# Kernel optimization log

Hardware: AMD Instinct MI355X
Metric: run time of the kernel (lower is better)

Reference implementation:

```python
import jax, jax.numpy as jnp
import numpy as np

B, T, D = 4, 2048, 1024

def layer_norm(x, gamma, bias):
    # NOTE: faithfully reproduces the source's (buggy) LN: x - mu/sqrt(var), unbiased var
    mu = jnp.mean(x, axis=-1, keepdims=True)
    var = jnp.var(x, axis=-1, ddof=1, keepdims=True)
    return (x - mu / jnp.sqrt(var)) * gamma + bias

def setup_inputs() -> dict:
    key = jax.random.key(0)
    ks = jax.random.split(key, 8)
    scale = 1.0 / np.sqrt(D)
    return {
        'x': jax.random.normal(ks[0], (B, T, D), dtype=jnp.float32),
        'gamma1': jnp.ones((D,), jnp.float32),
        'beta1': jnp.zeros((D,), jnp.float32),
        'w_q': jax.random.uniform(ks[1], (D, D), jnp.float32, -scale, scale),
        'w_k': jax.random.uniform(ks[2], (D, D), jnp.float32, -scale, scale),
        'w_v': jax.random.uniform(ks[3], (D, D), jnp.float32, -scale, scale),
        'gamma2': jnp.ones((D,), jnp.float32),
        'beta2': jnp.zeros((D,), jnp.float32),
        'W1': jax.random.uniform(ks[4], (D, D), jnp.float32, -scale, scale),
        'b1': jnp.zeros((D,), jnp.float32),
        'W2': jax.random.uniform(ks[5], (D, D), jnp.float32, -scale, scale),
        'b2': jnp.zeros((D,), jnp.float32),
    }

def reference(x, gamma1, beta1, w_q, w_k, w_v, gamma2, beta2, W1, b1, W2, b2):
    d_model = x.shape[-1]
    t = x.shape[1]
    h = layer_norm(x, gamma1, beta1)
    q = jnp.einsum('btk,kd->btd', h, w_q)
    k = jnp.einsum('btk,kd->btd', h, w_k)
    v = jnp.einsum('btk,kd->btd', h, w_v)
    scale = 1.0 / jnp.sqrt(jnp.asarray(d_model, x.dtype))
    causal = jnp.tril(jnp.ones((t, t), dtype=bool))
    mask = jnp.where(causal, 0.0, -jnp.inf).astype(x.dtype)
    scores = jnp.einsum('bqd,bkd->bqk', q, k) * scale + mask
    attn = jax.nn.softmax(scores, axis=-1)
    y = jnp.einsum('bqt,btd->bqd', attn, v) + x
    h2 = layer_norm(y, gamma2, beta2)
    out = jnp.maximum(h2 @ W1 + b1, 0.0) @ W2 + b2
    return out + y
```

## Files before the change

kernel.cpp:

```cpp
#include <hip/hip_runtime.h>
#include <hip/hip_bf16.h>
#include <math.h>

using bf16 = __hip_bfloat16;

static constexpr int Bn = 4;
static constexpr int Tn = 2048;
static constexpr int Dn = 1024;

typedef __attribute__((ext_vector_type(8))) short bf16x8;
typedef __attribute__((ext_vector_type(4))) float f32x4;

__device__ __forceinline__ float ldf(float v) { return v; }
__device__ __forceinline__ float ldf(bf16 v) { return __bfloat162float(v); }
__device__ __forceinline__ bf16 f2b(float v) { return __float2bfloat16(v); }
__device__ __forceinline__ float b2f(short s) {
    return __uint_as_float(((unsigned)(unsigned short)s) << 16);
}
__device__ __forceinline__ short f2bs(float v) {
    bf16 t = __float2bfloat16(v);
    return *reinterpret_cast<short*>(&t);
}

template <typename T> __device__ __forceinline__ T from_float(float v);
template <> __device__ __forceinline__ float from_float<float>(float v) { return v; }
template <> __device__ __forceinline__ bf16 from_float<bf16>(float v) { return f2b(v); }

__device__ __forceinline__ void load4(const float* p, float* v) {
    const float4 t = *(const float4*)p;
    v[0] = t.x; v[1] = t.y; v[2] = t.z; v[3] = t.w;
}
__device__ __forceinline__ void load4(const bf16* p, float* v) {
    const short4 t = *(const short4*)p;
    v[0] = b2f(t.x); v[1] = b2f(t.y); v[2] = b2f(t.z); v[3] = b2f(t.w);
}

__device__ __forceinline__ void async_copy16(const bf16* g, bf16* l) {
    __builtin_amdgcn_global_load_lds(
        (const __attribute__((address_space(1))) void*)g,
        (__attribute__((address_space(3))) void*)l,
        16, 0, 0);
}

template <int BM, int BN, int MINW, int EPI, typename OutT, typename ResT, bool RELU>
__global__ __launch_bounds__(256, MINW) void gemm_nt(
    const bf16* __restrict__ A, const bf16* __restrict__ Bm,
    OutT* __restrict__ C, const float* __restrict__ bias,
    const ResT* __restrict__ res, bf16* __restrict__ vtp,
    float* __restrict__ rowsum,
    int M, int N, int K, int lda, int ldb, int ldc,
    long sA, long sB, long sC, long sR, int mode)
{
    const int bm = blockIdx.x, bn = blockIdx.y, bz = blockIdx.z;
    if (mode == 1 && bn * BN > bm * BM + (BM - 1)) return;
    const int kend = bm * BM + BM;
    const int kmax = (mode == 2) ? (kend < K ? kend : K) : K;

    const bf16* Ab = A + (size_t)bz * sA;
    const bf16* Bb = Bm + (size_t)bz * sB;

    constexpr int WROWS = BM / 64;
    constexpr int WCOLS = 4 / WROWS;
    constexpr int TM = 64;
    constexpr int TN = BN / WCOLS;
    constexpr int MT = TM / 16;
    constexpr int NT = TN / 16;
    constexpr int nA = BM / 16;
    constexpr int nB = BN / 16;
    constexpr int TSTR = 132;
    constexpr int STAGE = 2 * (BM + BN) * 32;
    constexpr int SME = (EPI == 1 && BM * TSTR > STAGE) ? BM * TSTR : STAGE;

    __shared__ __align__(16) bf16 smem[SME];
    bf16* As = smem;
    bf16* Bs = smem + 2 * BM * 32;

    const int tid = threadIdx.x;
    const int wave = tid >> 6;
    const int lane = tid & 63;
    const int wm = wave / WCOLS;
    const int wn = wave % WCOLS;

    f32x4 acc[MT][NT] = {};

    const int lr = lane >> 2;
    const int lc = (lane & 3) * 8;
    const bf16* gAc[nA / 4]; bf16* lAc[nA / 4];
    const bf16* gBc[nB / 4]; bf16* lBc[nB / 4];
#pragma unroll
    for (int i = 0; i < nA / 4; ++i) {
        const int c = wave + 4 * i;
        gAc[i] = Ab + (size_t)(bm * BM + c * 16 + lr) * lda + lc;
        lAc[i] = &As[c * 512];
    }
#pragma unroll
    for (int i = 0; i < nB / 4; ++i) {
        const int c = wave + 4 * i;
        gBc[i] = Bb + (size_t)(bn * BN + c * 16 + lr) * ldb + lc;
        lBc[i] = &Bs[c * 512];
    }

    const int arow = lane & 15;
    const int kq = (lane >> 4) * 8;

    for (int k0 = 0; k0 < kmax; k0 += 64) {
#pragma unroll
        for (int hh = 0; hh < 2; ++hh) {
#pragma unroll
            for (int i = 0; i < nA / 4; ++i)
                async_copy16(gAc[i] + k0 + 32 * hh, lAc[i] + hh * (BM * 32));
#pragma unroll
            for (int i = 0; i < nB / 4; ++i)
                async_copy16(gBc[i] + k0 + 32 * hh, lBc[i] + hh * (BN * 32));
        }
        __syncthreads();

#pragma unroll
        for (int hh = 0; hh < 2; ++hh) {
            const bf16* Ah = As + hh * (BM * 32);
            const bf16* Bh = Bs + hh * (BN * 32);
            bf16x8 af[MT], bfm[NT];
#pragma unroll
            for (int t = 0; t < MT; ++t)
                af[t] = *(const bf16x8*)&Ah[(wm * TM + t * 16 + arow) * 32 + kq];
#pragma unroll
            for (int t = 0; t < NT; ++t)
                bfm[t] = *(const bf16x8*)&Bh[(wn * TN + t * 16 + arow) * 32 + kq];
#pragma unroll
            for (int mt = 0; mt < MT; ++mt)
#pragma unroll
                for (int nt = 0; nt < NT; ++nt)
                    acc[mt][nt] = __builtin_amdgcn_mfma_f32_16x16x32_bf16(
                        af[mt], bfm[nt], acc[mt][nt], 0, 0, 0);
        }
        __syncthreads();
    }

    const int rowBase = bm * BM + wm * TM;
    const int colBase = bn * BN + wn * TN;
    const int qrow = (lane >> 4) * 4;
    const int ccol = lane & 15;

    if (EPI == 1 && bn * BN >= 2048) {
        bf16* tt = smem;
#pragma unroll
        for (int mt = 0; mt < MT; ++mt) {
            const int tl = wm * TM + mt * 16 + qrow;
#pragma unroll
            for (int nt = 0; nt < NT; ++nt) {
                const int dl = wn * TN + nt * 16 + ccol;
                short4 o;
                o.x = f2bs(acc[mt][nt][0]);
                o.y = f2bs(acc[mt][nt][1]);
                o.z = f2bs(acc[mt][nt][2]);
                o.w = f2bs(acc[mt][nt][3]);
                *(short4*)&tt[dl * TSTR + tl] = o;
            }
        }
        __syncthreads();
        const int dl = tid >> 1;
        const int th = (tid & 1) * 64;
        const int dg = bn * BN - 2048 + dl;
        const int b = (bm * BM) >> 11;
        const int tin = (bm * BM) & (Tn - 1);
        bf16* dst = vtp + ((size_t)b * Dn + dg) * Tn + tin + th;
        const bf16* srcl = &tt[dl * TSTR + th];
#pragma unroll
        for (int i = 0; i < 16; ++i)
            ((short4*)dst)[i] = ((const short4*)srcl)[i];
        return;
    }

    if (EPI == 2) {
        OutT* Cb = C + (size_t)bz * sC;
        float* rsb = rowsum + (size_t)bz * Tn;
        const float scale = 0.03125f;
#pragma unroll
        for (int mt = 0; mt < MT; ++mt) {
            float rsv[4] = {0.f, 0.f, 0.f, 0.f};
#pragma unroll
            for (int nt = 0; nt < NT; ++nt) {
                const int cc = colBase + nt * 16 + ccol;
#pragma unroll
                for (int r = 0; r < 4; ++r) {
                    const int rr = rowBase + mt * 16 + qrow + r;
                    float e = 0.0f;
                    if (cc <= rr) {
                        const short es = f2bs(__expf(acc[mt][nt][r] * scale));
                        Cb[(size_t)rr * ldc + cc] = *(const bf16*)&es;
                        e = b2f(es);
                    } else {
                        Cb[(size_t)rr * ldc + cc] = from_float<OutT>(0.0f);
                    }
                    rsv[r] += e;
                }
            }
#pragma unroll
            for (int r = 0; r < 4; ++r) {
                float v = rsv[r];
                v += __shfl_xor(v, 1);
                v += __shfl_xor(v, 2);
                v += __shfl_xor(v, 4);
                v += __shfl_xor(v, 8);
                if (ccol == 0)
                    atomicAdd(rsb + rowBase + mt * 16 + qrow + r, v);
            }
        }
        return;
    }

    OutT* Cb = C + (size_t)bz * sC;
    const ResT* Rb = res ? (res + (size_t)bz * sR) : nullptr;
    const float* rsb = (EPI == 3) ? (rowsum + (size_t)bz * Tn) : nullptr;
#pragma unroll
    for (int mt = 0; mt < MT; ++mt) {
        float inv4[4];
        if (EPI == 3) {
#pragma unroll
            for (int r = 0; r < 4; ++r)
                inv4[r] = 1.0f / rsb[rowBase + mt * 16 + qrow + r];
        }
#pragma unroll
        for (int nt = 0; nt < NT; ++nt) {
            const int cc = colBase + nt * 16 + ccol;
            const float bv = bias ? bias[cc] : 0.0f;
#pragma unroll
            for (int r = 0; r < 4; ++r) {
                const int rr = rowBase + mt * 16 + qrow + r;
                float v = acc[mt][nt][r];
                if (EPI == 3) v *= inv4[r];
                v += bv;
                if (RELU) v = fmaxf(v, 0.0f);
                if (Rb) v += ldf(Rb[(size_t)rr * ldc + cc]);
                Cb[(size_t)rr * ldc + cc] = from_float<OutT>(v);
            }
        }
    }
}

template <typename InT>
__device__ __forceinline__ void ln_row(
    const InT* __restrict__ xr, const float* __restrict__ gamma,
    const float* __restrict__ beta, bf16* __restrict__ orow, int tid)
{
    const int j = tid * 4;
    float v[4];
    load4(xr + j, v);
    float s = v[0] + v[1] + v[2] + v[3];
    float sq = v[0] * v[0] + v[1] * v[1] + v[2] * v[2] + v[3] * v[3];
#pragma unroll
    for (int o = 32; o > 0; o >>= 1) {
        s += __shfl_down(s, o);
        sq += __shfl_down(sq, o);
    }
    __shared__ float red[2][4];
    const int lane = tid & 63, w = tid >> 6;
    if (lane == 0) { red[0][w] = s; red[1][w] = sq; }
    __syncthreads();
    s  = red[0][0] + red[0][1] + red[0][2] + red[0][3];
    sq = red[1][0] + red[1][1] + red[1][2] + red[1][3];
    const float mean = s / (float)Dn;
    const float var = (sq - s * s / (float)Dn) / (float)(Dn - 1);
    const float coef = mean * rsqrtf(var);

    const float4 g = *(const float4*)(gamma + j);
    const float4 be = *(const float4*)(beta + j);
    short4 o;
    o.x = f2bs((v[0] - coef) * g.x + be.x);
    o.y = f2bs((v[1] - coef) * g.y + be.y);
    o.z = f2bs((v[2] - coef) * g.z + be.z);
    o.w = f2bs((v[3] - coef) * g.w + be.w);
    *(short4*)(orow + j) = o;
}

template <typename InT>
__global__ __launch_bounds__(256) void ln_kernel(
    const InT* __restrict__ x, const float* __restrict__ gamma,
    const float* __restrict__ beta, bf16* __restrict__ out)
{
    const int row = blockIdx.x;
    ln_row(x + (size_t)row * Dn, gamma, beta, out + (size_t)row * Dn, threadIdx.x);
}

struct WPtrs { const float* p[5]; };

__global__ __launch_bounds__(256) void prep_kernel(
    WPtrs wp, bf16* __restrict__ wdst, float* __restrict__ rowsum,
    const float* __restrict__ x, const float* __restrict__ gamma1,
    const float* __restrict__ beta1, bf16* __restrict__ h)
{
    const int bx = blockIdx.x;
    if (bx < 5120) {
        __shared__ bf16 tile[32][33];
        const int z = bx >> 10;
        const int t = bx & 1023;
        const float* src = wp.p[z];
        bf16* d = wdst + (size_t)z * Dn * Dn;
        const int c0 = (t & 31) * 32, r0 = (t >> 5) * 32;
        const int tx = threadIdx.x & 31;
        const int ty = threadIdx.x >> 5;
#pragma unroll
        for (int dy = 0; dy < 32; dy += 8)
            tile[ty + dy][tx] = f2b(src[(size_t)(r0 + ty + dy) * Dn + (c0 + tx)]);
        __syncthreads();
#pragma unroll
        for (int dy = 0; dy < 32; dy += 8)
            d[(size_t)(c0 + ty + dy) * Dn + (r0 + tx)] = tile[tx][ty + dy];
    } else if (bx < 5128) {
        const int idx = (bx - 5120) * 1024 + (int)threadIdx.x;
        const int base = (bx - 5120) * 1024;
#pragma unroll
        for (int i = 0; i < 4; ++i) rowsum[base + i * 256 + threadIdx.x] = 0.0f;
        (void)idx;
    } else {
        const int row = bx - 5128;
        ln_row(x + (size_t)row * Dn, gamma1, beta1, h + (size_t)row * Dn, threadIdx.x);
    }
}

extern "C" void kernel_launch(void* const* d_in, const int* in_sizes, int n_in,
                              void* d_out, int out_size, void* d_ws, size_t ws_size,
                              hipStream_t stream) {
    const float* x      = (const float*)d_in[0];
    const float* gamma1 = (const float*)d_in[1];
    const float* beta1  = (const float*)d_in[2];
    const float* w_q    = (const float*)d_in[3];
    const float* w_k    = (const float*)d_in[4];
    const float* w_v    = (const float*)d_in[5];
    const float* gamma2 = (const float*)d_in[6];
    const float* beta2  = (const float*)d_in[7];
    const float* W1     = (const float*)d_in[8];
    const float* b1     = (const float*)d_in[9];
    const float* W2     = (const float*)d_in[10];
    const float* b2     = (const float*)d_in[11];
    float* out = (float*)d_out;

    char* ws = (char*)d_ws;
    size_t off = 0;
    auto alloc = [&](size_t bytes) {
        char* p = ws + off;
        off += (bytes + 255) & ~(size_t)255;
        return p;
    };
    const size_t BT = (size_t)Bn * Tn;
    bf16* h    = (bf16*)alloc(BT * Dn * 2);
    bf16* qk   = (bf16*)alloc(BT * 2 * Dn * 2);
    bf16* vt   = (bf16*)alloc(BT * Dn * 2);
    bf16* wbuf = (bf16*)alloc((size_t)5 * Dn * Dn * 2);
    bf16* S    = (bf16*)alloc((size_t)Bn * Tn * Tn * 2);
    bf16* y    = (bf16*)alloc(BT * Dn * 2);
    float* rowsum = (float*)alloc((size_t)Bn * Tn * 4);
    bf16* h2   = h;
    bf16* mid  = qk;

    const dim3 blk(256);
    const long TD  = (long)Tn * Dn;
    const long TT  = (long)Tn * Tn;
    const long TD2 = (long)Tn * 2 * Dn;

    WPtrs wp; wp.p[0] = w_q; wp.p[1] = w_k; wp.p[2] = w_v; wp.p[3] = W1; wp.p[4] = W2;
    prep_kernel<<<dim3(5128 + (unsigned)BT, 1, 1), blk, 0, stream>>>(
        wp, wbuf, rowsum, x, gamma1, beta1, h);

    gemm_nt<128, 128, 4, 1, bf16, float, false><<<dim3(64, 24, 1), blk, 0, stream>>>(
        h, wbuf, qk, nullptr, nullptr, vt, nullptr,
        (int)BT, 3 * Dn, Dn, Dn, Dn, 2 * Dn, 0, 0, 0, 0, 0);

    gemm_nt<128, 128, 4, 2, bf16, float, false><<<dim3(16, 16, Bn), blk, 0, stream>>>(
        qk, qk + 1024, S, nullptr, nullptr, nullptr, rowsum,
        Tn, Tn, Dn, 2 * Dn, 2 * Dn, Tn, TD2, TD2, TT, 0, 1);

    gemm_nt<128, 128, 4, 3, bf16, float, false><<<dim3(16, 8, Bn), blk, 0, stream>>>(
        S, vt, y, nullptr, x, nullptr, rowsum,
        Tn, Dn, Tn, Tn, Tn, Dn, TT, TD, TD, TD, 2);

    ln_kernel<bf16><<<dim3((unsigned)BT), blk, 0, stream>>>(y, gamma2, beta2, h2);

    gemm_nt<128, 128, 4, 0, bf16, float, true><<<dim3(64, 8, 1), blk, 0, stream>>>(
        h2, wbuf + (size_t)3 * Dn * Dn, mid, b1, nullptr, nullptr, nullptr,
        (int)BT, Dn, Dn, Dn, Dn, Dn, 0, 0, 0, 0, 0);

    gemm_nt<128, 128, 4, 0, float, bf16, false><<<dim3(64, 8, 1), blk, 0, stream>>>(
        mid, wbuf + (size_t)4 * Dn * Dn, out, b2, y, nullptr, nullptr,
        (int)BT, Dn, Dn, Dn, Dn, Dn, 0, 0, 0, 0, 0);
}
```

Baseline: 353.5 us.

## Split QKV projection into 256x256 triple-buffered QK GEMM and transposed V GEMM

Replaces the single fused QKV GEMM, whose epilogue transposed V through shared memory, with two launches. A new 512-thread 256x256-tile kernel computes Q and K using a triple-buffered async global-to-LDS pipeline, split MFMA phases and priority hints. V^T is produced directly by a second GEMM with swapped operands (W_v^T times h per batch), so the transpose epilogue and its extra shared memory are removed. This adds a launch and relies on the hand-written wait counts and barriers in the new pipeline being correct.

```diff
diff --git a/kernel.cpp b/kernel.cpp
--- a/kernel.cpp
+++ b/kernel.cpp
@@ -40,6 +40,129 @@
         (const __attribute__((address_space(1))) void*)g,
         (__attribute__((address_space(3))) void*)l,
         16, 0, 0);
+}
+
+__global__ __launch_bounds__(512, 2) void gemm8p(
+    const bf16* __restrict__ A, const bf16* __restrict__ Bm,
+    bf16* __restrict__ C, int K, int lda, int ldb, int ldc)
+{
+    constexpr int BM = 256, BN = 256, BK = 32;
+    constexpr int BUFE = (BM + BN) * BK;
+    __shared__ __align__(16) bf16 smem[3 * BUFE];
+
+    const int bm = blockIdx.x, bn = blockIdx.y;
+    const int tid = threadIdx.x;
+    const int wave = tid >> 6;
+    const int lane = tid & 63;
+    const int wm = wave >> 2;
+    const int wn = wave & 3;
+    const int lr = lane >> 2;
+    const int lc = (lane & 3) * 8;
+    const int arow = lane & 15;
+    const int kq = (lane >> 4) * 8;
+
+    const int NK = K / BK;
+
+    const bf16* gA0 = A + (size_t)(bm * BM + wave * 16 + lr) * lda + lc;
+    const bf16* gA1 = A + (size_t)(bm * BM + (wave + 8) * 16 + lr) * lda + lc;
+    const bf16* gB0 = Bm + (size_t)(bn * BN + wave * 16 + lr) * ldb + lc;
+    const bf16* gB1 = Bm + (size_t)(bn * BN + (wave + 8) * 16 + lr) * ldb + lc;
+
+    f32x4 acc[8][4] = {};
+
+    {
+        bf16* As0 = smem;
+        bf16* Bs0 = smem + BM * BK;
+        bf16* As1 = smem + BUFE;
+        bf16* Bs1 = smem + BUFE + BM * BK;
+        async_copy16(gA0, As0 + wave * 512);
+        async_copy16(gA1, As0 + (wave + 8) * 512);
+        async_copy16(gB0, Bs0 + wave * 512);
+        async_copy16(gB1, Bs0 + (wave + 8) * 512);
+        async_copy16(gA0 + BK, As1 + wave * 512);
+        async_copy16(gA1 + BK, As1 + (wave + 8) * 512);
+        async_copy16(gB0 + BK, Bs1 + wave * 512);
+        async_copy16(gB1 + BK, Bs1 + (wave + 8) * 512);
+    }
+    asm volatile("s_waitcnt vmcnt(4)" ::: "memory");
+    __builtin_amdgcn_s_barrier();
+
+    int cb = 0;
+    int sb = 2;
+    for (int kt = 0; kt < NK; ++kt) {
+        const bf16* As = smem + cb * BUFE;
+        const bf16* Bs = As + BM * BK;
+        const bool st = (kt + 2) < NK;
+        const int koff = (kt + 2) * BK;
+
+        bf16x8 af[8], bf0[2];
+#pragma unroll
+        for (int mt = 0; mt < 8; ++mt)
+            af[mt] = *(const bf16x8*)&As[(wm * 8 + mt) * 512 + arow * 32 + kq];
+#pragma unroll
+        for (int nt = 0; nt < 2; ++nt)
+            bf0[nt] = *(const bf16x8*)&Bs[(wn * 4 + nt) * 512 + arow * 32 + kq];
+        if (st) {
+            bf16* Ad = smem + sb * BUFE;
+            async_copy16(gA0 + koff, Ad + wave * 512);
+            async_copy16(gA1 + koff, Ad + (wave + 8) * 512);
+        }
+        __builtin_amdgcn_s_barrier();
+        asm volatile("s_waitcnt lgkmcnt(0)" ::: "memory");
+        __builtin_amdgcn_sched_barrier(0);
+        __builtin_amdgcn_s_setprio(1);
+#pragma unroll
+        for (int mt = 0; mt < 8; ++mt)
+#pragma unroll
+            for (int nt = 0; nt < 2; ++nt)
+                acc[mt][nt] = __builtin_amdgcn_mfma_f32_16x16x32_bf16(
+                    af[mt], bf0[nt], acc[mt][nt], 0, 0, 0);
+        __builtin_amdgcn_s_setprio(0);
+        __builtin_amdgcn_s_barrier();
+
+        bf16x8 bf1[2];
+#pragma unroll
+        for (int nt = 0; nt < 2; ++nt)
+            bf1[nt] = *(const bf16x8*)&Bs[(wn * 4 + 2 + nt) * 512 + arow * 32 + kq];
+        if (st) {
+            bf16* Bd = smem + sb * BUFE + BM * BK;
+            async_copy16(gB0 + koff, Bd + wave * 512);
+            async_copy16(gB1 + koff, Bd + (wave + 8) * 512);
+        }
+        __builtin_amdgcn_s_barrier();
+        asm volatile("s_waitcnt lgkmcnt(0)" ::: "memory");
+        __builtin_amdgcn_sched_barrier(0);
+        __builtin_amdgcn_s_setprio(1);
+#pragma unroll
+        for (int mt = 0; mt < 8; ++mt)
+#pragma unroll
+            for (int nt = 0; nt < 2; ++nt)
+                acc[mt][2 + nt] = __builtin_amdgcn_mfma_f32_16x16x32_bf16(
+                    af[mt], bf1[nt], acc[mt][2 + nt], 0, 0, 0);
+        __builtin_amdgcn_s_setprio(0);
+        if (st) asm volatile("s_waitcnt vmcnt(4)" ::: "memory");
+        else    asm volatile("s_waitcnt vmcnt(0)" ::: "memory");
+        __builtin_amdgcn_s_barrier();
+
+        cb = (cb + 1 == 3) ? 0 : cb + 1;
+        sb = (sb + 1 == 3) ? 0 : sb + 1;
+    }
+
+    const int row0 = bm * BM + wm * 128;
+    const int col0 = bn * BN + wn * 64;
+    const int qrow = (lane >> 4) * 4;
+    const int ccol = lane & 15;
+#pragma unroll
+    for (int mt = 0; mt < 8; ++mt)
+#pragma unroll
+        for (int nt = 0; nt < 4; ++nt) {
+            const int cc = col0 + nt * 16 + ccol;
+#pragma unroll
+            for (int r = 0; r < 4; ++r) {
+                const int rr = row0 + mt * 16 + qrow + r;
+                C[(size_t)rr * ldc + cc] = f2b(acc[mt][nt][r]);
+            }
+        }
 }
 
 template <int BM, int BN, int MINW, int EPI, typename OutT, typename ResT, bool RELU>
@@ -67,11 +190,9 @@
     constexpr int NT = TN / 16;
     constexpr int nA = BM / 16;
     constexpr int nB = BN / 16;
-    constexpr int TSTR = 132;
     constexpr int STAGE = 2 * (BM + BN) * 32;
-    constexpr int SME = (EPI == 1 && BM * TSTR > STAGE) ? BM * TSTR : STAGE;
-
-    __shared__ __align__(16) bf16 smem[SME];
+
+    __shared__ __align__(16) bf16 smem[STAGE];
     bf16* As = smem;
     bf16* Bs = smem + 2 * BM * 32;
 
@@ -140,36 +261,6 @@
     const int colBase = bn * BN + wn * TN;
     const int qrow = (lane >> 4) * 4;
     const int ccol = lane & 15;
-
-    if (EPI == 1 && bn * BN >= 2048) {
-        bf16* tt = smem;
-#pragma unroll
-        for (int mt = 0; mt < MT; ++mt) {
-            const int tl = wm * TM + mt * 16 + qrow;
-#pragma unroll
-            for (int nt = 0; nt < NT; ++nt) {
-                const int dl = wn * TN + nt * 16 + ccol;
-                short4 o;
-                o.x = f2bs(acc[mt][nt][0]);
-                o.y = f2bs(acc[mt][nt][1]);
-                o.z = f2bs(acc[mt][nt][2]);
-                o.w = f2bs(acc[mt][nt][3]);
-                *(short4*)&tt[dl * TSTR + tl] = o;
-            }
-        }
-        __syncthreads();
-        const int dl = tid >> 1;
-        const int th = (tid & 1) * 64;
-        const int dg = bn * BN - 2048 + dl;
-        const int b = (bm * BM) >> 11;
-        const int tin = (bm * BM) & (Tn - 1);
-        bf16* dst = vtp + ((size_t)b * Dn + dg) * Tn + tin + th;
-        const bf16* srcl = &tt[dl * TSTR + th];
-#pragma unroll
-        for (int i = 0; i < 16; ++i)
-            ((short4*)dst)[i] = ((const short4*)srcl)[i];
-        return;
-    }
 
     if (EPI == 2) {
         OutT* Cb = C + (size_t)bz * sC;
@@ -307,11 +398,9 @@
         for (int dy = 0; dy < 32; dy += 8)
             d[(size_t)(c0 + ty + dy) * Dn + (r0 + tx)] = tile[tx][ty + dy];
     } else if (bx < 5128) {
-        const int idx = (bx - 5120) * 1024 + (int)threadIdx.x;
         const int base = (bx - 5120) * 1024;
 #pragma unroll
         for (int i = 0; i < 4; ++i) rowsum[base + i * 256 + threadIdx.x] = 0.0f;
-        (void)idx;
     } else {
         const int row = bx - 5128;
         ln_row(x + (size_t)row * Dn, gamma1, beta1, h + (size_t)row * Dn, threadIdx.x);
@@ -362,9 +451,12 @@
     prep_kernel<<<dim3(5128 + (unsigned)BT, 1, 1), blk, 0, stream>>>(
         wp, wbuf, rowsum, x, gamma1, beta1, h);
 
-    gemm_nt<128, 128, 4, 1, bf16, float, false><<<dim3(64, 24, 1), blk, 0, stream>>>(
-        h, wbuf, qk, nullptr, nullptr, vt, nullptr,
-        (int)BT, 3 * Dn, Dn, Dn, Dn, 2 * Dn, 0, 0, 0, 0, 0);
+    gemm8p<<<dim3(32, 8, 1), dim3(512), 0, stream>>>(
+        h, wbuf, qk, Dn, Dn, Dn, 2 * Dn);
+
+    gemm_nt<128, 128, 4, 0, bf16, float, false><<<dim3(8, 16, Bn), blk, 0, stream>>>(
+        wbuf + (size_t)2 * Dn * Dn, h, vt, nullptr, nullptr, nullptr, nullptr,
+        Dn, Tn, Dn, Dn, Dn, Tn, 0, TD, (long)Dn * Tn, 0, 0);
 
     gemm_nt<128, 128, 4, 2, bf16, float, false><<<dim3(16, 16, Bn), blk, 0, stream>>>(
         qk, qk + 1024, S, nullptr, nullptr, nullptr, rowsum,
```

Measured after the change: 353.1 us. No clear change (-0.1%).
